# Performance work log

Hardware: AMD Instinct MI355X
Metric: run time of the kernel (lower is better)

The kernel has to match this reference:

```python
import jax, jax.numpy as jnp
import numpy as np

INF = 99999.0  # sentinel used by the original torch module


def _dtw_table(x, y):
    """Full (N+1, M+1) DTW DP table, identical math to the torch double loop.

    Row recurrence: r[j+1] = c[j] + min(prev[j+1], prev[j], r[j]).
    Rewritten as the min-plus linear recurrence r[j+1] = min(a[j] + r[j], b[j])
    with a[j] = c[j], b[j] = c[j] + min(prev[j+1], prev[j]), which is
    associative and solved per-row with lax.associative_scan (wavefront-free
    parallelism within each row); rows advance with lax.scan.
    """
    M = y.shape[0]
    dt = x.dtype
    row0 = jnp.full((M + 1,), INF, dtype=dt).at[0].set(0.0)  # dtw[0, :]
    inf1 = jnp.full((1,), INF, dtype=dt)

    def combine(l, r):
        a1, b1 = l
        a2, b2 = r
        return (a1 + a2, jnp.minimum(a2 + b1, b2))

    def step(prev, xi):
        c = (xi - y) ** 2                              # (M,) squared cost
        m = jnp.minimum(prev[1:], prev[:-1])           # min(dtw[i,j+1], dtw[i,j])
        A, B = jax.lax.associative_scan(combine, (c, c + m))
        r = jnp.minimum(A + INF, B)                    # r[0] = INF folded in
        row = jnp.concatenate([inf1, r])               # dtw[i+1, :]
        return row, row

    _, rows = jax.lax.scan(step, row0, x)              # (N, M+1)
    table = jnp.concatenate([row0[None, :], rows], axis=0)
    return jnp.sqrt(table)


def setup_inputs() -> dict:
    key = jax.random.key(0)
    kx, ky = jax.random.split(key)
    N = M = 6144
    x = jax.random.normal(kx, (N,), dtype=jnp.float32)
    y = jax.random.normal(ky, (M,), dtype=jnp.float32)
    return {"x": x, "y": y}


def reference(x, y):
    return _dtw_table(x, y)
```

## Files before the change

### kernel.cpp

```cpp
#include <hip/hip_runtime.h>
#include <math.h>

#define NN    6144
#define MP1   6145
#define FINF  99999.0f

#define R1     8
#define KC1    8
#define WCH1   (KC1 * 64)
#define GCH1   (NN / WCH1)
#define RTS1   8
#define NWS1   (NN / R1)
#define STEPS1 (NWS1 + 63)

#define R2     4
#define KC2    8
#define WCH2   (KC2 * 64)
#define BR     384
#define NBI    (NN / BR)
#define TS2    (BR / R2)
#define STEPS2 (TS2 + 63)

typedef float f4a __attribute__((ext_vector_type(4), aligned(4)));
typedef float f4v __attribute__((ext_vector_type(4), aligned(16)));

__device__ __forceinline__ float readlane_f(float v, int l) {
    return __int_as_float(__builtin_amdgcn_readlane(__float_as_int(v), l));
}
__device__ __forceinline__ float shup1(float v) {
    return __int_as_float(__builtin_amdgcn_update_dpp(
        0, __float_as_int(v), 0x138, 0xF, 0xF, false));
}

__global__ void __launch_bounds__(64) dtw_bnd(const float* __restrict__ x,
                                              const float* __restrict__ y,
                                              int* __restrict__ flags,
                                              float* __restrict__ bnd,
                                              float* __restrict__ rowb) {
    const int g    = blockIdx.x;
    const int lane = threadIdx.x;
    const int c0   = g * WCH1 + lane * KC1;

    float yv[KC1], cur[KC1];
#pragma unroll
    for (int q = 0; q < KC1; ++q) {
        yv[q]  = y[c0 + q];
        cur[q] = FINF;
    }
    float pl = (c0 == 0) ? 0.0f : FINF;
    float rlast[R1];
#pragma unroll
    for (int r = 0; r < R1; ++r) rlast[r] = FINF;
    float vbuf = FINF, vnext = FINF;

    const float4* x4 = (const float4*)x;
    float4 xwA  = x4[2 * lane];
    float4 xwB  = x4[2 * lane + 1];
    float4 xwAN = x4[2 * (64 + lane)];
    float4 xwBN = x4[2 * (64 + lane) + 1];
    float xcur[R1];
#pragma unroll
    for (int r = 0; r < R1; ++r) xcur[r] = x[r];

    float cnx[R1][KC1];
#pragma unroll
    for (int r = 0; r < R1; ++r)
#pragma unroll
        for (int q = 0; q < KC1; ++q) {
            const float d = xcur[r] - yv[q];
            cnx[r][q] = d * d;
        }

    if (g != 0) {
        while (__hip_atomic_load(&flags[(g - 1) * 16], __ATOMIC_ACQUIRE,
                                 __HIP_MEMORY_SCOPE_AGENT) < 1) {
            __builtin_amdgcn_s_sleep(1);
        }
        vnext = bnd[(size_t)(g - 1) * NN + lane];
    }

    for (int s = 0; s < STEPS1; ++s) {
        if (g != GCH1 - 1 && s > 64 && ((s - 64) & (RTS1 - 1)) == 0) {
            if (lane == 0)
                __hip_atomic_store(&flags[g * 16], (s - 64) >> 3,
                                   __ATOMIC_RELEASE, __HIP_MEMORY_SCOPE_AGENT);
        }

        if (g != 0 && s < NWS1 && (s & (RTS1 - 1)) == 0) vbuf = vnext;

        if (g != 0 && (s & (RTS1 - 1)) == RTS1 - 4 && (s + 4) < NWS1) {
            const int want = ((s + 4) >> 3) + 1;
            while (__hip_atomic_load(&flags[(g - 1) * 16], __ATOMIC_ACQUIRE,
                                     __HIP_MEMORY_SCOPE_AGENT) < want) {
                __builtin_amdgcn_s_sleep(1);
            }
            vnext = bnd[(size_t)(g - 1) * NN + (size_t)R1 * (s + 4) + lane];
        }

        float vin[R1];
#pragma unroll
        for (int r = 0; r < R1; ++r) {
            const float up = shup1(rlast[r]);
            const float vb = readlane_f(vbuf, ((s & (RTS1 - 1)) << 3) + r);
            const float l0 = (g == 0) ? FINF : vb;
            vin[r] = (lane == 0) ? l0 : up;
        }

        const int  t      = s - lane;
        const bool active = (t >= 0) && (t < NWS1);
        if (active) {
#pragma unroll
            for (int r = 0; r < R1; ++r) {
                float rl  = vin[r];
                float pm1 = (r == 0) ? pl : vin[r - 1];
                float nv[KC1];
#pragma unroll
                for (int q = 0; q < KC1; ++q) {
                    const float upv = cur[q];
                    rl     = cnx[r][q] + fminf(fminf(rl, upv), pm1);
                    pm1    = upv;
                    cur[q] = rl;
                    nv[q]  = rl;
                }
                rlast[r] = rl;
                if (r == R1 - 1) {
                    const int tp1 = t + 1;
                    const int k   = tp1 / 48;
                    if (k * 48 == tp1 && k >= 1 && k <= NBI - 1) {
                        *(f4a*)&rowb[(size_t)k * MP1 + c0 + 1] =
                            (f4a){nv[0], nv[1], nv[2], nv[3]};
                        *(f4a*)&rowb[(size_t)k * MP1 + c0 + 5] =
                            (f4a){nv[4], nv[5], nv[6], nv[7]};
                    }
                }
            }
            pl = vin[R1 - 1];
            if (lane == 63) {
                *(f4v*)&bnd[(size_t)g * NN + (size_t)R1 * t] =
                    (f4v){rlast[0], rlast[1], rlast[2], rlast[3]};
                *(f4v*)&bnd[(size_t)g * NN + (size_t)R1 * t + 4] =
                    (f4v){rlast[4], rlast[5], rlast[6], rlast[7]};
            }
        }

        const int sn = s + 1;
        if ((sn & 63) == 0) {
            xwA = xwAN;
            xwB = xwBN;
            int nb = sn + 64 + lane;
            if (nb > NN / 8 - 1) nb = NN / 8 - 1;
            xwAN = x4[2 * nb];
            xwBN = x4[2 * nb + 1];
        }
        const float* xap = (const float*)&xwA;
        const float* xbp = (const float*)&xwB;
#pragma unroll
        for (int r = 0; r < 4; ++r) {
            const float xs = shup1(xcur[r]);
            const float xj = readlane_f(xap[r], sn & 63);
            xcur[r] = (lane == 0) ? xj : xs;
        }
#pragma unroll
        for (int r = 4; r < 8; ++r) {
            const float xs = shup1(xcur[r]);
            const float xj = readlane_f(xbp[r - 4], sn & 63);
            xcur[r] = (lane == 0) ? xj : xs;
        }
#pragma unroll
        for (int r = 0; r < R1; ++r)
#pragma unroll
            for (int q = 0; q < KC1; ++q) {
                const float d = xcur[r] - yv[q];
                cnx[r][q] = d * d;
            }
    }

    if (g != GCH1 - 1 && lane == 0) {
        __hip_atomic_store(&flags[g * 16], NWS1 >> 3,
                           __ATOMIC_RELEASE, __HIP_MEMORY_SCOPE_AGENT);
    }
}

__global__ void __launch_bounds__(64) dtw_tile(const float* __restrict__ x,
                                               const float* __restrict__ y,
                                               const float* __restrict__ bnd,
                                               const float* __restrict__ rowb,
                                               float* __restrict__ out) {
    const int bj   = blockIdx.x;
    const int bi   = blockIdx.y;
    const int lane = threadIdx.x;

    __shared__ float left_s[BR];
    __shared__ float top_s[WCH2 + 1];
    __shared__ float xb_s[BR];

#pragma unroll
    for (int k = 0; k < BR / 64; ++k) {
        const int i = 64 * k + lane;
        left_s[i] = (bj == 0) ? FINF
                              : bnd[(size_t)(bj - 1) * NN + BR * bi + i];
        xb_s[i] = x[BR * bi + i];
    }
    for (int c = lane; c < WCH2 + 1; c += 64) {
        float tv;
        if (bi == 0)                tv = (bj == 0 && c == 0) ? 0.0f : FINF;
        else if (c == 0 && bj == 0) tv = FINF;
        else                        tv = rowb[(size_t)bi * MP1 + WCH2 * bj + c];
        top_s[c] = tv;
    }
    __syncthreads();

    const int c0 = WCH2 * bj + KC2 * lane;
    float yv[KC2], cur[KC2];
#pragma unroll
    for (int q = 0; q < KC2; ++q) {
        yv[q]  = y[c0 + q];
        cur[q] = top_s[KC2 * lane + q + 1];
    }
    float pl = top_s[KC2 * lane];
    float rlast[R2];
#pragma unroll
    for (int r = 0; r < R2; ++r) rlast[r] = FINF;

    float xcur[R2];
#pragma unroll
    for (int r = 0; r < R2; ++r) xcur[r] = xb_s[r];
    float cnx[R2][KC2];
#pragma unroll
    for (int r = 0; r < R2; ++r)
#pragma unroll
        for (int q = 0; q < KC2; ++q) {
            const float d = xcur[r] - yv[q];
            cnx[r][q] = d * d;
        }

    int off = (BR * bi + 1 - R2 * lane) * MP1 + c0 + 1;

    for (int s = 0; s < STEPS2; ++s) {
        float vin[R2];
#pragma unroll
        for (int r = 0; r < R2; ++r) {
            const float up = shup1(rlast[r]);
            const int  li  = R2 * s + r;
            const float l0 = left_s[li < BR ? li : BR - 1];
            vin[r] = (lane == 0) ? l0 : up;
        }

        const int  t      = s - lane;
        const bool active = (t >= 0) && (t < TS2);
        if (active) {
#pragma unroll
            for (int r = 0; r < R2; ++r) {
                float rl  = vin[r];
                float pm1 = (r == 0) ? pl : vin[r - 1];
                float nv[KC2];
#pragma unroll
                for (int q = 0; q < KC2; ++q) {
                    const float upv = cur[q];
                    rl     = cnx[r][q] + fminf(fminf(rl, upv), pm1);
                    pm1    = upv;
                    cur[q] = rl;
                    nv[q]  = rl;
                }
                rlast[r] = rl;
                *(f4a*)(&out[off + r * MP1]) =
                    (f4a){__builtin_amdgcn_sqrtf(nv[0]),
                          __builtin_amdgcn_sqrtf(nv[1]),
                          __builtin_amdgcn_sqrtf(nv[2]),
                          __builtin_amdgcn_sqrtf(nv[3])};
                *(f4a*)(&out[off + r * MP1 + 4]) =
                    (f4a){__builtin_amdgcn_sqrtf(nv[4]),
                          __builtin_amdgcn_sqrtf(nv[5]),
                          __builtin_amdgcn_sqrtf(nv[6]),
                          __builtin_amdgcn_sqrtf(nv[7])};
            }
            pl = vin[R2 - 1];
        }
        off += R2 * MP1;

        const int sn = s + 1;
#pragma unroll
        for (int r = 0; r < R2; ++r) {
            const float xs = shup1(xcur[r]);
            const int  xi  = R2 * sn + r;
            const float xj = xb_s[xi < BR ? xi : BR - 1];
            xcur[r] = (lane == 0) ? xj : xs;
        }
#pragma unroll
        for (int r = 0; r < R2; ++r)
#pragma unroll
            for (int q = 0; q < KC2; ++q) {
                const float d = xcur[r] - yv[q];
                cnx[r][q] = d * d;
            }
    }
}

__global__ void dtw_edges(float* __restrict__ out, float ev) {
    const int idx = blockIdx.x * blockDim.x + threadIdx.x;
    if (idx <= NN) {
        out[idx] = (idx == 0) ? 0.0f : ev;
        if (idx >= 1) out[(size_t)idx * MP1] = ev;
    }
}

extern "C" void kernel_launch(void* const* d_in, const int* in_sizes, int n_in,
                              void* d_out, int out_size, void* d_ws, size_t ws_size,
                              hipStream_t stream) {
    (void)in_sizes; (void)n_in; (void)out_size; (void)ws_size;
    const float* x = (const float*)d_in[0];
    const float* y = (const float*)d_in[1];
    float* out     = (float*)d_out;
    int* flags     = (int*)d_ws;

    const size_t bnd_off  = 4096;
    const size_t bnd_sz   = (size_t)GCH1 * NN * sizeof(float);
    const size_t rowb_off = bnd_off + bnd_sz;
    float* bnd  = (float*)((char*)d_ws + bnd_off);
    float* rowb = (float*)((char*)d_ws + rowb_off);

    hipMemsetAsync(flags, 0, GCH1 * 16 * sizeof(int), stream);

    dtw_edges<<<(MP1 + 255) / 256, 256, 0, stream>>>(out, sqrtf(FINF));
    dtw_bnd<<<GCH1, 64, 0, stream>>>(x, y, flags, bnd, rowb);
    dtw_tile<<<dim3(GCH1, NBI), 64, 0, stream>>>(x, y, bnd, rowb, out);
}
```

Before: 1.571 ms.

## Traverse per-thread DTW sub-tile in anti-diagonal order and compute costs inline

Both kernels now walk each thread's R×KC cell block in anti-diagonal order instead of row-by-row. Cells on the same diagonal are independent, which shortens the serial dependency chain of min/add operations and exposes instruction-level parallelism. The precomputed squared-cost array is dropped and costs are computed inline, which cuts register pressure at the price of recomputing the subtraction and multiply. The tile kernel buffers all results in nvm before storing, which may add registers.

Measured after the change: 1.687 ms. 7.4% more time.

```diff
diff --git a/kernel.cpp b/kernel.cpp
--- a/kernel.cpp
+++ b/kernel.cpp
@@ -48,9 +48,9 @@
         cur[q] = FINF;
     }
     float pl = (c0 == 0) ? 0.0f : FINF;
-    float rlast[R1];
-#pragma unroll
-    for (int r = 0; r < R1; ++r) rlast[r] = FINF;
+    float rowval[R1];
+#pragma unroll
+    for (int r = 0; r < R1; ++r) rowval[r] = FINF;
     float vbuf = FINF, vnext = FINF;
 
     const float4* x4 = (const float4*)x;
@@ -62,15 +62,6 @@
 #pragma unroll
     for (int r = 0; r < R1; ++r) xcur[r] = x[r];
 
-    float cnx[R1][KC1];
-#pragma unroll
-    for (int r = 0; r < R1; ++r)
-#pragma unroll
-        for (int q = 0; q < KC1; ++q) {
-            const float d = xcur[r] - yv[q];
-            cnx[r][q] = d * d;
-        }
-
     if (g != 0) {
         while (__hip_atomic_load(&flags[(g - 1) * 16], __ATOMIC_ACQUIRE,
                                  __HIP_MEMORY_SCOPE_AGENT) < 1) {
@@ -100,7 +91,7 @@
         float vin[R1];
 #pragma unroll
         for (int r = 0; r < R1; ++r) {
-            const float up = shup1(rlast[r]);
+            const float up = shup1(rowval[r]);
             const float vb = readlane_f(vbuf, ((s & (RTS1 - 1)) << 3) + r);
             const float l0 = (g == 0) ? FINF : vb;
             vin[r] = (lane == 0) ? l0 : up;
@@ -109,37 +100,45 @@
         const int  t      = s - lane;
         const bool active = (t >= 0) && (t < NWS1);
         if (active) {
-#pragma unroll
-            for (int r = 0; r < R1; ++r) {
-                float rl  = vin[r];
-                float pm1 = (r == 0) ? pl : vin[r - 1];
-                float nv[KC1];
-#pragma unroll
-                for (int q = 0; q < KC1; ++q) {
-                    const float upv = cur[q];
-                    rl     = cnx[r][q] + fminf(fminf(rl, upv), pm1);
-                    pm1    = upv;
-                    cur[q] = rl;
-                    nv[q]  = rl;
+            float rv[R1], rd[R1];
+#pragma unroll
+            for (int r = 0; r < R1; ++r) rv[r] = vin[r];
+
+#pragma unroll
+            for (int d = 0; d < R1 + KC1 - 1; ++d) {
+#pragma unroll
+                for (int r = R1 - 1; r >= 0; --r) {
+                    const int q = d - r;
+                    if (q < 0 || q >= KC1) continue;
+                    const float up = (r == 0) ? cur[q] : rv[r - 1];
+                    const float dg = (r == 0) ? ((q == 0) ? pl : cur[q - 1])
+                                              : rd[r - 1];
+                    const float dx = xcur[r] - yv[q];
+                    const float nv = dx * dx + fminf(fminf(up, dg), rv[r]);
+                    rd[r] = rv[r];
+                    rv[r] = nv;
+                    if (r == R1 - 1) cur[q] = nv;
                 }
-                rlast[r] = rl;
-                if (r == R1 - 1) {
-                    const int tp1 = t + 1;
-                    const int k   = tp1 / 48;
-                    if (k * 48 == tp1 && k >= 1 && k <= NBI - 1) {
-                        *(f4a*)&rowb[(size_t)k * MP1 + c0 + 1] =
-                            (f4a){nv[0], nv[1], nv[2], nv[3]};
-                        *(f4a*)&rowb[(size_t)k * MP1 + c0 + 5] =
-                            (f4a){nv[4], nv[5], nv[6], nv[7]};
-                    }
+            }
+#pragma unroll
+            for (int r = 0; r < R1; ++r) rowval[r] = rv[r];
+            pl = vin[R1 - 1];
+
+            {
+                const int tp1 = t + 1;
+                const int k   = tp1 / 48;
+                if (k * 48 == tp1 && k >= 1 && k <= NBI - 1) {
+                    *(f4a*)&rowb[(size_t)k * MP1 + c0 + 1] =
+                        (f4a){cur[0], cur[1], cur[2], cur[3]};
+                    *(f4a*)&rowb[(size_t)k * MP1 + c0 + 5] =
+                        (f4a){cur[4], cur[5], cur[6], cur[7]};
                 }
             }
-            pl = vin[R1 - 1];
             if (lane == 63) {
                 *(f4v*)&bnd[(size_t)g * NN + (size_t)R1 * t] =
-                    (f4v){rlast[0], rlast[1], rlast[2], rlast[3]};
+                    (f4v){rowval[0], rowval[1], rowval[2], rowval[3]};
                 *(f4v*)&bnd[(size_t)g * NN + (size_t)R1 * t + 4] =
-                    (f4v){rlast[4], rlast[5], rlast[6], rlast[7]};
+                    (f4v){rowval[4], rowval[5], rowval[6], rowval[7]};
             }
         }
 
@@ -166,13 +165,6 @@
             const float xj = readlane_f(xbp[r - 4], sn & 63);
             xcur[r] = (lane == 0) ? xj : xs;
         }
-#pragma unroll
-        for (int r = 0; r < R1; ++r)
-#pragma unroll
-            for (int q = 0; q < KC1; ++q) {
-                const float d = xcur[r] - yv[q];
-                cnx[r][q] = d * d;
-            }
     }
 
     if (g != GCH1 - 1 && lane == 0) {
@@ -225,14 +217,6 @@
     float xcur[R2];
 #pragma unroll
     for (int r = 0; r < R2; ++r) xcur[r] = xb_s[r];
-    float cnx[R2][KC2];
-#pragma unroll
-    for (int r = 0; r < R2; ++r)
-#pragma unroll
-        for (int q = 0; q < KC2; ++q) {
-            const float d = xcur[r] - yv[q];
-            cnx[r][q] = d * d;
-        }
 
     int off = (BR * bi + 1 - R2 * lane) * MP1 + c0 + 1;
 
@@ -249,32 +233,44 @@
         const int  t      = s - lane;
         const bool active = (t >= 0) && (t < TS2);
         if (active) {
+            float rv[R2], rd[R2], nvm[R2][KC2];
+#pragma unroll
+            for (int r = 0; r < R2; ++r) rv[r] = vin[r];
+
+#pragma unroll
+            for (int d = 0; d < R2 + KC2 - 1; ++d) {
+#pragma unroll
+                for (int r = R2 - 1; r >= 0; --r) {
+                    const int q = d - r;
+                    if (q < 0 || q >= KC2) continue;
+                    const float up = (r == 0) ? cur[q] : rv[r - 1];
+                    const float dg = (r == 0) ? ((q == 0) ? pl : cur[q - 1])
+                                              : rd[r - 1];
+                    const float dx = xcur[r] - yv[q];
+                    const float nv = dx * dx + fminf(fminf(up, dg), rv[r]);
+                    rd[r] = rv[r];
+                    rv[r] = nv;
+                    nvm[r][q] = nv;
+                    if (r == R2 - 1) cur[q] = nv;
+                }
+            }
+#pragma unroll
+            for (int r = 0; r < R2; ++r) rlast[r] = rv[r];
+            pl = vin[R2 - 1];
+
 #pragma unroll
             for (int r = 0; r < R2; ++r) {
-                float rl  = vin[r];
-                float pm1 = (r == 0) ? pl : vin[r - 1];
-                float nv[KC2];
-#pragma unroll
-                for (int q = 0; q < KC2; ++q) {
-                    const float upv = cur[q];
-                    rl     = cnx[r][q] + fminf(fminf(rl, upv), pm1);
-                    pm1    = upv;
-                    cur[q] = rl;
-                    nv[q]  = rl;
-                }
-                rlast[r] = rl;
                 *(f4a*)(&out[off + r * MP1]) =
-                    (f4a){__builtin_amdgcn_sqrtf(nv[0]),
-                          __builtin_amdgcn_sqrtf(nv[1]),
-                          __builtin_amdgcn_sqrtf(nv[2]),
-                          __builtin_amdgcn_sqrtf(nv[3])};
+                    (f4a){__builtin_amdgcn_sqrtf(nvm[r][0]),
+                          __builtin_amdgcn_sqrtf(nvm[r][1]),
+                          __builtin_amdgcn_sqrtf(nvm[r][2]),
+                          __builtin_amdgcn_sqrtf(nvm[r][3])};
                 *(f4a*)(&out[off + r * MP1 + 4]) =
-                    (f4a){__builtin_amdgcn_sqrtf(nv[4]),
-                          __builtin_amdgcn_sqrtf(nv[5]),
-                          __builtin_amdgcn_sqrtf(nv[6]),
-                          __builtin_amdgcn_sqrtf(nv[7])};
-            }
-            pl = vin[R2 - 1];
+                    (f4a){__builtin_amdgcn_sqrtf(nvm[r][4]),
+                          __builtin_amdgcn_sqrtf(nvm[r][5]),
+                          __builtin_amdgcn_sqrtf(nvm[r][6]),
+                          __builtin_amdgcn_sqrtf(nvm[r][7])};
+            }
         }
         off += R2 * MP1;
 
@@ -286,13 +282,6 @@
             const float xj = xb_s[xi < BR ? xi : BR - 1];
             xcur[r] = (lane == 0) ? xj : xs;
         }
-#pragma unroll
-        for (int r = 0; r < R2; ++r)
-#pragma unroll
-            for (int q = 0; q < KC2; ++q) {
-                const float d = xcur[r] - yv[q];
-                cnx[r][q] = d * d;
-            }
     }
 }
 
```
